# Kernel optimization log

Hardware: AMD Instinct MI355X
Metric: run time of the kernel (lower is better)

Reference implementation:

```python
import jax, jax.numpy as jnp
import numpy as np

IN_OCT = 512
OUT_OCT = 512
BATCH = 512


def setup_inputs() -> dict:
    key = jax.random.key(0)
    kx, kw = jax.random.split(key)
    x = jax.random.normal(kx, (BATCH, IN_OCT * 8), dtype=jnp.float32)
    weight = jax.random.normal(kw, (OUT_OCT, IN_OCT, 8, 8), dtype=jnp.float32)
    bias = jnp.zeros((OUT_OCT, 8), dtype=jnp.float32)
    return {"x": x, "weight": weight, "bias": bias}


def reference(x, weight, bias):
    # x: [B, in_oct*8]; weight: [out_oct, in_oct, 8, 8]; bias: [out_oct, 8]
    B = x.shape[0]
    out_oct, in_oct = weight.shape[0], weight.shape[1]
    xo = x.reshape(B, in_oct, 8)
    # octonion_mul(x[:, j], weight[i, j]) applies the per-pair 8x8 octonion
    # left-multiplication matrix; summed over j it is one bilinear contraction.
    y = jnp.einsum("bjp,ijpk->bik", xo, weight) + bias[None, :, :]
    return y.reshape(B, out_oct * 8)
```

## Files before the change

kernel.cpp:

```cpp
#include <hip/hip_runtime.h>
#include <stdint.h>


#define M_DIM 512
#define N_DIM 4096
#define K_DIM 4096
#define KSPLIT 4

typedef __bf16 bf16x8 __attribute__((ext_vector_type(8)));
typedef float f32x4 __attribute__((ext_vector_type(4)));

__device__ inline unsigned short f2bf(float f) {
  union { float f; unsigned int u; } v;
  v.f = f;
  unsigned int u = v.u;
  unsigned int r = (u + 0x7fffu + ((u >> 16) & 1u)) >> 16;
  return (unsigned short)r;
}

__global__ __launch_bounds__(256) void prep_kernel(
    const float* __restrict__ x, const float* __restrict__ w,
    const float* __restrict__ bias, unsigned short* __restrict__ abf,
    unsigned short* __restrict__ bt, float* __restrict__ out) {
  const int bid = blockIdx.x;
  const int tid = threadIdx.x;
  if (bid < 8192) {
    int g = bid * 256 + tid;
    int k = g & 7;
    int j = (g >> 3) & 511;
    int i = g >> 12;
    const float* wb = w + ((size_t)(i * 512 + j) * 64 + k);
    __attribute__((aligned(16))) unsigned short o[8];
#pragma unroll
    for (int p = 0; p < 8; ++p) o[p] = f2bf(wb[p * 8]);
    *(uint4*)(bt + (size_t)(i * 8 + k) * K_DIM + j * 8) = *(const uint4*)o;
  } else if (bid < 9216) {
    int g = (bid - 8192) * 256 + tid;
    const float4* xi = (const float4*)x;
    float4 a = xi[g * 2];
    float4 b = xi[g * 2 + 1];
    __attribute__((aligned(16))) unsigned short o[8] = {
        f2bf(a.x), f2bf(a.y), f2bf(a.z), f2bf(a.w),
        f2bf(b.x), f2bf(b.y), f2bf(b.z), f2bf(b.w)};
    *(uint4*)(abf + (size_t)g * 8) = *(const uint4*)o;
  } else {
    int g = (bid - 9216) * 256 + tid;
    int el = g * 4;
    int col = el & (N_DIM - 1);
    *(float4*)(out + el) = *(const float4*)(bias + col);
  }
}

__device__ inline void gld16(const void* g, void* l) {
  __builtin_amdgcn_global_load_lds(
      (const __attribute__((address_space(1))) unsigned int*)g,
      (__attribute__((address_space(3))) unsigned int*)l, 16, 0, 0);
}

__global__ __launch_bounds__(256) void gemm_kernel(
    const unsigned short* __restrict__ A, const unsigned short* __restrict__ Bt,
    float* __restrict__ out) {
  __shared__ __align__(16) unsigned short lA[128 * 32];
  __shared__ __align__(16) unsigned short lB[128 * 32];
  const int t = threadIdx.x;
  const int n0 = blockIdx.x * 128;
  const int m0 = blockIdx.y * 128;
  const int kc0 = blockIdx.z * (K_DIM / KSPLIT);
  const int w = t >> 6;
  const int lane = t & 63;
  const int wr = w >> 1;
  const int wc = w & 1;
  const int lrow = lane & 15;
  const int kb = lane >> 4;

  f32x4 acc[4][4] = {};

  const int s0 = t, s1 = t + 256;
  const int row0 = s0 >> 2, c0 = (s0 & 3) * 8;
  const int row1 = s1 >> 2, c1 = (s1 & 3) * 8;

  for (int it = 0; it < (K_DIM / KSPLIT) / 32; ++it) {
    const int kk = kc0 + it * 32;
    __syncthreads();
    gld16(A + (size_t)(m0 + row0) * K_DIM + kk + c0, (char*)lA + s0 * 16);
    gld16(Bt + (size_t)(n0 + row0) * K_DIM + kk + c0, (char*)lB + s0 * 16);
    gld16(A + (size_t)(m0 + row1) * K_DIM + kk + c1, (char*)lA + s1 * 16);
    gld16(Bt + (size_t)(n0 + row1) * K_DIM + kk + c1, (char*)lB + s1 * 16);
    __syncthreads();

    bf16x8 af[4], bfr[4];
#pragma unroll
    for (int mt = 0; mt < 4; ++mt)
      af[mt] = *(const bf16x8*)(lA + (wr * 64 + mt * 16 + lrow) * 32 + kb * 8);
#pragma unroll
    for (int nt = 0; nt < 4; ++nt)
      bfr[nt] = *(const bf16x8*)(lB + (wc * 64 + nt * 16 + lrow) * 32 + kb * 8);
#pragma unroll
    for (int mt = 0; mt < 4; ++mt)
#pragma unroll
      for (int nt = 0; nt < 4; ++nt)
        acc[mt][nt] = __builtin_amdgcn_mfma_f32_16x16x32_bf16(
            af[mt], bfr[nt], acc[mt][nt], 0, 0, 0);
  }

#pragma unroll
  for (int mt = 0; mt < 4; ++mt) {
    const int gmb = m0 + wr * 64 + mt * 16 + kb * 4;
#pragma unroll
    for (int nt = 0; nt < 4; ++nt) {
      const int gn = n0 + wc * 64 + nt * 16 + lrow;
#pragma unroll
      for (int r = 0; r < 4; ++r)
        atomicAdd(out + (size_t)(gmb + r) * N_DIM + gn, acc[mt][nt][r]);
    }
  }
}

extern "C" void kernel_launch(void* const* d_in, const int* in_sizes, int n_in,
                              void* d_out, int out_size, void* d_ws,
                              size_t ws_size, hipStream_t stream) {
  const float* x = (const float*)d_in[0];
  const float* w = (const float*)d_in[1];
  const float* bias = (const float*)d_in[2];
  float* out = (float*)d_out;

  unsigned short* abf = (unsigned short*)d_ws;
  unsigned short* bt = abf + (size_t)M_DIM * K_DIM;

  prep_kernel<<<11264, 256, 0, stream>>>(x, w, bias, abf, bt, out);

  dim3 grid(N_DIM / 128, M_DIM / 128, KSPLIT);
  gemm_kernel<<<grid, 256, 0, stream>>>(abf, bt, out);
}
```

Before: 154.7 us.

## Double-buffer GEMM LDS tiles and transpose weights through LDS in prep

The GEMM now double-buffers its A and B LDS tiles. Each iteration issues the asynchronous global-to-LDS loads for the next K slice before running the MFMAs on the current one, leaving one barrier per iteration instead of two. The weight-prep path also changes: each block reads contiguous float4 chunks of the weight tensor, packs them to bf16 into an LDS transpose buffer, and writes full 16-byte row segments of the transposed matrix. Both changes aim to cut memory-latency stalls and scattered stores, at the cost of twice the GEMM LDS footprint, which may lower occupancy.

```diff
diff --git a/kernel.cpp b/kernel.cpp
--- a/kernel.cpp
+++ b/kernel.cpp
@@ -23,19 +23,40 @@
     const float* __restrict__ bias, unsigned short* __restrict__ abf,
     unsigned short* __restrict__ bt, float* __restrict__ out) {
   const int bid = blockIdx.x;
-  const int tid = threadIdx.x;
-  if (bid < 8192) {
-    int g = bid * 256 + tid;
-    int k = g & 7;
-    int j = (g >> 3) & 511;
-    int i = g >> 12;
-    const float* wb = w + ((size_t)(i * 512 + j) * 64 + k);
-    __attribute__((aligned(16))) unsigned short o[8];
+  const int t = threadIdx.x;
+  if (bid < 4096) {
+    __shared__ __align__(16) unsigned short lT[8][512];
+    const int i = bid >> 3;
+    const int jg = bid & 7;
+    const float4* src =
+        (const float4*)(w + (size_t)i * 32768 + jg * 4096 + t * 16);
+    float4 v0 = src[0], v1 = src[1], v2 = src[2], v3 = src[3];
+    const int jp = (t >> 2) * 8 + (t & 3) * 2;
+    unsigned int* dst32;
+    const float* lo = (const float*)&v0;
+    const float* hi = (const float*)&v2;
 #pragma unroll
-    for (int p = 0; p < 8; ++p) o[p] = f2bf(wb[p * 8]);
-    *(uint4*)(bt + (size_t)(i * 8 + k) * K_DIM + j * 8) = *(const uint4*)o;
-  } else if (bid < 9216) {
-    int g = (bid - 8192) * 256 + tid;
+    for (int k = 0; k < 4; ++k) {
+      unsigned int pk =
+          (unsigned int)f2bf(lo[k]) | ((unsigned int)f2bf(hi[k]) << 16);
+      *(unsigned int*)&lT[k][jp] = pk;
+    }
+    lo = (const float*)&v1;
+    hi = (const float*)&v3;
+#pragma unroll
+    for (int k = 0; k < 4; ++k) {
+      unsigned int pk =
+          (unsigned int)f2bf(lo[k]) | ((unsigned int)f2bf(hi[k]) << 16);
+      *(unsigned int*)&lT[k + 4][jp] = pk;
+    }
+    __syncthreads();
+    const int r = t >> 5, c = t & 31;
+    const uint4* s = (const uint4*)&lT[r][c * 16];
+    uint4* d = (uint4*)(bt + (size_t)(i * 8 + r) * K_DIM + jg * 512 + c * 16);
+    d[0] = s[0];
+    d[1] = s[1];
+  } else if (bid < 5120) {
+    int g = (bid - 4096) * 256 + t;
     const float4* xi = (const float4*)x;
     float4 a = xi[g * 2];
     float4 b = xi[g * 2 + 1];
@@ -44,7 +65,7 @@
         f2bf(b.x), f2bf(b.y), f2bf(b.z), f2bf(b.w)};
     *(uint4*)(abf + (size_t)g * 8) = *(const uint4*)o;
   } else {
-    int g = (bid - 9216) * 256 + tid;
+    int g = (bid - 5120) * 256 + t;
     int el = g * 4;
     int col = el & (N_DIM - 1);
     *(float4*)(out + el) = *(const float4*)(bias + col);
@@ -60,8 +81,8 @@
 __global__ __launch_bounds__(256) void gemm_kernel(
     const unsigned short* __restrict__ A, const unsigned short* __restrict__ Bt,
     float* __restrict__ out) {
-  __shared__ __align__(16) unsigned short lA[128 * 32];
-  __shared__ __align__(16) unsigned short lB[128 * 32];
+  __shared__ __align__(16) unsigned short lA[2][128 * 32];
+  __shared__ __align__(16) unsigned short lB[2][128 * 32];
   const int t = threadIdx.x;
   const int n0 = blockIdx.x * 128;
   const int m0 = blockIdx.y * 128;
@@ -78,23 +99,39 @@
   const int s0 = t, s1 = t + 256;
   const int row0 = s0 >> 2, c0 = (s0 & 3) * 8;
   const int row1 = s1 >> 2, c1 = (s1 & 3) * 8;
+  const size_t aO0 = (size_t)(m0 + row0) * K_DIM + c0;
+  const size_t aO1 = (size_t)(m0 + row1) * K_DIM + c1;
+  const size_t bO0 = (size_t)(n0 + row0) * K_DIM + c0;
+  const size_t bO1 = (size_t)(n0 + row1) * K_DIM + c1;
 
-  for (int it = 0; it < (K_DIM / KSPLIT) / 32; ++it) {
-    const int kk = kc0 + it * 32;
+  const int NIT = (K_DIM / KSPLIT) / 32;
+
+  gld16(A + aO0 + kc0, (char*)lA[0] + s0 * 16);
+  gld16(Bt + bO0 + kc0, (char*)lB[0] + s0 * 16);
+  gld16(A + aO1 + kc0, (char*)lA[0] + (s1 - 256) * 16 + 4096);
+  gld16(Bt + bO1 + kc0, (char*)lB[0] + (s1 - 256) * 16 + 4096);
+
+  for (int it = 0; it < NIT; ++it) {
     __syncthreads();
-    gld16(A + (size_t)(m0 + row0) * K_DIM + kk + c0, (char*)lA + s0 * 16);
-    gld16(Bt + (size_t)(n0 + row0) * K_DIM + kk + c0, (char*)lB + s0 * 16);
-    gld16(A + (size_t)(m0 + row1) * K_DIM + kk + c1, (char*)lA + s1 * 16);
-    gld16(Bt + (size_t)(n0 + row1) * K_DIM + kk + c1, (char*)lB + s1 * 16);
-    __syncthreads();
+    if (it + 1 < NIT) {
+      const int kk = kc0 + (it + 1) * 32;
+      char* dA = (char*)lA[(it + 1) & 1];
+      char* dB = (char*)lB[(it + 1) & 1];
+      gld16(A + aO0 + kk, dA + s0 * 16);
+      gld16(Bt + bO0 + kk, dB + s0 * 16);
+      gld16(A + aO1 + kk, dA + (s1 - 256) * 16 + 4096);
+      gld16(Bt + bO1 + kk, dB + (s1 - 256) * 16 + 4096);
+    }
+    const unsigned short* cA = lA[it & 1];
+    const unsigned short* cB = lB[it & 1];
 
     bf16x8 af[4], bfr[4];
 #pragma unroll
     for (int mt = 0; mt < 4; ++mt)
-      af[mt] = *(const bf16x8*)(lA + (wr * 64 + mt * 16 + lrow) * 32 + kb * 8);
+      af[mt] = *(const bf16x8*)(cA + (wr * 64 + mt * 16 + lrow) * 32 + kb * 8);
 #pragma unroll
     for (int nt = 0; nt < 4; ++nt)
-      bfr[nt] = *(const bf16x8*)(lB + (wc * 64 + nt * 16 + lrow) * 32 + kb * 8);
+      bfr[nt] = *(const bf16x8*)(cB + (wc * 64 + nt * 16 + lrow) * 32 + kb * 8);
 #pragma unroll
     for (int mt = 0; mt < 4; ++mt)
 #pragma unroll
@@ -127,7 +164,7 @@
   unsigned short* abf = (unsigned short*)d_ws;
   unsigned short* bt = abf + (size_t)M_DIM * K_DIM;
 
-  prep_kernel<<<11264, 256, 0, stream>>>(x, w, bias, abf, bt, out);
+  prep_kernel<<<7168, 256, 0, stream>>>(x, w, bias, abf, bt, out);
 
   dim3 grid(N_DIM / 128, M_DIM / 128, KSPLIT);
   gemm_kernel<<<grid, 256, 0, stream>>>(abf, bt, out);
```

Result: no change. 155.7 us (+0.6%).
